# Kernel optimization log

Hardware: AMD Instinct MI355X
Metric: run time of the kernel (lower is better)

The kernel has to match this reference:

```python
import jax, jax.numpy as jnp
import numpy as np

BETA = 100.0


def setup_inputs() -> dict:
    key = jax.random.key(0)
    k1, k2 = jax.random.split(key)
    E, d, N = 1250000, 64, 50000
    M = jax.random.normal(k1, (E, d), dtype=jnp.float32)
    dest = jax.random.randint(k2, (E,), 0, N, dtype=jnp.int32)
    return {"M": M, "dest": dest, "dim_size": N}


def reference(M, dest, dim_size):
    # scatter_max over dim 0: per-node elementwise max of incoming messages -> [N, d]
    M_v = jax.ops.segment_max(M, dest, num_segments=dim_size)
    # scatter_softmax(M * BETA, dest): segment-wise stable softmax along dim 0
    logits = M * BETA  # [E, d]
    seg_max = jax.ops.segment_max(logits, dest, num_segments=dim_size)  # [N, d]
    z = jnp.exp(logits - seg_max[dest])  # [E, d]
    denom = jax.ops.segment_sum(z, dest, num_segments=dim_size)  # [N, d]
    w = (z / denom[dest])[:, None, :]  # unsqueeze(1) -> [E, 1, d]
    return (M_v, w)
```

## Files before the change

### kernel.cpp

```cpp
#include <hip/hip_runtime.h>
#include <cmath>

#define BETA 100.0f
#define CAP 80


__global__ void k_zero1(int* __restrict__ p, int n) {
    int i = blockIdx.x * blockDim.x + threadIdx.x;
    if (i < n) p[i] = 0;
}

__global__ void k_place(const int* __restrict__ dest, int* __restrict__ cursor,
                        int* __restrict__ bucket, int e, int cap) {
    int i = blockIdx.x * blockDim.x + threadIdx.x;
    if (i < e) {
        int d = dest[i];
        int pos = atomicAdd(&cursor[d], 1);
        if (pos < cap) bucket[d * cap + pos] = i;
    }
}

#define SCAN_B 128
#define SCAN_T 256

__global__ void k_zero(int* __restrict__ cnt, int* __restrict__ cursor, int n) {
    int i = blockIdx.x * blockDim.x + threadIdx.x;
    if (i < n) { cnt[i] = 0; cursor[i] = 0; }
}

__global__ void k_hist(const int* __restrict__ dest, int* __restrict__ cnt, int e) {
    int i = blockIdx.x * blockDim.x + threadIdx.x;
    if (i < e) atomicAdd(&cnt[dest[i]], 1);
}

__global__ void __launch_bounds__(SCAN_T) k_scan1(const int* __restrict__ cnt,
                                                  int* __restrict__ partial, int n) {
    int b = blockIdx.x, tid = threadIdx.x;
    int per_b = (n + SCAN_B - 1) / SCAN_B;
    int bs = b * per_b;
    int be = bs + per_b; if (be > n) be = n;
    int sum = 0;
    for (int i = bs + tid; i < be; i += SCAN_T) sum += cnt[i];
    __shared__ int lds[SCAN_T];
    lds[tid] = sum;
    __syncthreads();
    for (int off = SCAN_T >> 1; off > 0; off >>= 1) {
        if (tid < off) lds[tid] += lds[tid + off];
        __syncthreads();
    }
    if (tid == 0) partial[b] = lds[0];
}

__global__ void __launch_bounds__(SCAN_B) k_scan2(int* __restrict__ partial) {
    int tid = threadIdx.x;
    __shared__ int lds[SCAN_B];
    int v = partial[tid];
    lds[tid] = v;
    __syncthreads();
    for (int off = 1; off < SCAN_B; off <<= 1) {
        int t = (tid >= off) ? lds[tid - off] : 0;
        __syncthreads();
        lds[tid] += t;
        __syncthreads();
    }
    partial[tid] = lds[tid] - v;
}

__global__ void __launch_bounds__(SCAN_T) k_scan3(const int* __restrict__ cnt,
                                                  const int* __restrict__ partial,
                                                  int* __restrict__ offs, int n) {
    int b = blockIdx.x, tid = threadIdx.x;
    int per_b = (n + SCAN_B - 1) / SCAN_B;
    int bs = b * per_b;
    int be = bs + per_b; if (be > n) be = n;
    int per_t = (per_b + SCAN_T - 1) / SCAN_T;
    int ts = bs + tid * per_t;
    int te = ts + per_t; if (te > be) te = be;
    int sum = 0;
    for (int i = ts; i < te; ++i) sum += cnt[i];
    __shared__ int lds[SCAN_T];
    lds[tid] = sum;
    __syncthreads();
    for (int off = 1; off < SCAN_T; off <<= 1) {
        int t = (tid >= off) ? lds[tid - off] : 0;
        __syncthreads();
        lds[tid] += t;
        __syncthreads();
    }
    int run = partial[b] + lds[tid] - sum;
    for (int i = ts; i < te; ++i) { offs[i] = run; run += cnt[i]; }
}

__global__ void k_bucket(const int* __restrict__ dest, const int* __restrict__ offs,
                         int* __restrict__ cursor, int* __restrict__ bucket, int e) {
    int i = blockIdx.x * blockDim.x + threadIdx.x;
    if (i < e) {
        int d = dest[i];
        int pos = atomicAdd(&cursor[d], 1);
        bucket[offs[d] + pos] = i;
    }
}

__global__ void __launch_bounds__(256) k_node(const float4* __restrict__ M4,
                                              const int* __restrict__ cnt,
                                              const int* __restrict__ offs,
                                              const int* __restrict__ bucket,
                                              float4* __restrict__ mv4,
                                              float4* __restrict__ w4, int n, int stride) {
    int tid = threadIdx.x;
    int node = blockIdx.x * 4 + (tid >> 6);
    if (node >= n) return;
    int lane = tid & 63;
    int g = lane >> 4;
    int q = lane & 15;
    int count = cnt[node];
    int base;
    if (stride > 0) {
        if (count > stride) count = stride;
        base = node * stride;
    } else {
        base = offs[node];
    }

    if (count == 0) {
        if (g == 0) mv4[(size_t)node * 16 + q] =
            make_float4(-INFINITY, -INFINITY, -INFINITY, -INFINITY);
        return;
    }

    if (count <= 64) {
        int eL = bucket[base + (lane < count ? lane : 0)];

        float4 mx = make_float4(-INFINITY, -INFINITY, -INFINITY, -INFINITY);
        float4 s = make_float4(0.f, 0.f, 0.f, 0.f);
        #pragma unroll 2
        for (int j = 0; j < count; j += 4) {
            int jj = j + g;
            bool act = jj < count;
            int e = __shfl(eL, act ? jj : 0);
            float4 v = M4[(size_t)e * 16 + q];
            if (act) {
                float nm;
                nm = fmaxf(mx.x, v.x);
                s.x = s.x * __expf(BETA * (mx.x - nm)) + __expf(BETA * (v.x - nm));
                mx.x = nm;
                nm = fmaxf(mx.y, v.y);
                s.y = s.y * __expf(BETA * (mx.y - nm)) + __expf(BETA * (v.y - nm));
                mx.y = nm;
                nm = fmaxf(mx.z, v.z);
                s.z = s.z * __expf(BETA * (mx.z - nm)) + __expf(BETA * (v.z - nm));
                mx.z = nm;
                nm = fmaxf(mx.w, v.w);
                s.w = s.w * __expf(BETA * (mx.w - nm)) + __expf(BETA * (v.w - nm));
                mx.w = nm;
            }
        }
        #pragma unroll
        for (int off = 16; off <= 32; off <<= 1) {
            float om, os, nm;
            om = __shfl_xor(mx.x, off); os = __shfl_xor(s.x, off);
            nm = fmaxf(mx.x, om);
            s.x = s.x * __expf(BETA * (mx.x - nm)) + os * __expf(BETA * (om - nm));
            mx.x = nm;
            om = __shfl_xor(mx.y, off); os = __shfl_xor(s.y, off);
            nm = fmaxf(mx.y, om);
            s.y = s.y * __expf(BETA * (mx.y - nm)) + os * __expf(BETA * (om - nm));
            mx.y = nm;
            om = __shfl_xor(mx.z, off); os = __shfl_xor(s.z, off);
            nm = fmaxf(mx.z, om);
            s.z = s.z * __expf(BETA * (mx.z - nm)) + os * __expf(BETA * (om - nm));
            mx.z = nm;
            om = __shfl_xor(mx.w, off); os = __shfl_xor(s.w, off);
            nm = fmaxf(mx.w, om);
            s.w = s.w * __expf(BETA * (mx.w - nm)) + os * __expf(BETA * (om - nm));
            mx.w = nm;
        }
        float4 inv;
        inv.x = __builtin_amdgcn_rcpf(s.x);
        inv.y = __builtin_amdgcn_rcpf(s.y);
        inv.z = __builtin_amdgcn_rcpf(s.z);
        inv.w = __builtin_amdgcn_rcpf(s.w);

        #pragma unroll 2
        for (int j = 0; j < count; j += 4) {
            int jj = j + g;
            bool act = jj < count;
            int e = __shfl(eL, act ? jj : 0);
            float4 v = M4[(size_t)e * 16 + q];
            if (act) {
                float4 o;
                o.x = __expf(BETA * (v.x - mx.x)) * inv.x;
                o.y = __expf(BETA * (v.y - mx.y)) * inv.y;
                o.z = __expf(BETA * (v.z - mx.z)) * inv.z;
                o.w = __expf(BETA * (v.w - mx.w)) * inv.w;
                w4[(size_t)e * 16 + q] = o;
            }
        }
        if (g == 0) mv4[(size_t)node * 16 + q] = mx;
    } else {
        const float* M = (const float*)M4;
        float* mv = (float*)mv4;
        float* w = (float*)w4;
        float mxs = -INFINITY;
        for (int j = 0; j < count; ++j) {
            int e = bucket[base + j];
            mxs = fmaxf(mxs, M[(size_t)e * 64 + lane]);
        }
        float ss = 0.f;
        for (int j = 0; j < count; ++j) {
            int e = bucket[base + j];
            ss += __expf(BETA * (M[(size_t)e * 64 + lane] - mxs));
        }
        float invs = __builtin_amdgcn_rcpf(ss);
        for (int j = 0; j < count; ++j) {
            int e = bucket[base + j];
            float x = M[(size_t)e * 64 + lane];
            w[(size_t)e * 64 + lane] = __expf(BETA * (x - mxs)) * invs;
        }
        mv[(size_t)node * 64 + lane] = mxs;
    }
}

extern "C" void kernel_launch(void* const* d_in, const int* in_sizes, int n_in,
                              void* d_out, int out_size, void* d_ws, size_t ws_size,
                              hipStream_t stream) {
    const float* M = (const float*)d_in[0];
    const int* dest = (const int*)d_in[1];
    const int E = in_sizes[1];
    const int d = in_sizes[0] / E;
    const int N = (out_size - in_sizes[0]) / d;

    float* mv = (float*)d_out;
    float* w = (float*)d_out + (size_t)N * d;

    const int B = 256;
    size_t need_fast = ((size_t)N * (CAP + 1)) * sizeof(int);

    if (ws_size >= need_fast) {
        int* cursor = (int*)d_ws;
        int* bucket = cursor + N;
        hipLaunchKernelGGL(k_zero1, dim3((N + B - 1) / B), dim3(B), 0, stream, cursor, N);
        hipLaunchKernelGGL(k_place, dim3((E + B - 1) / B), dim3(B), 0, stream,
                           dest, cursor, bucket, E, CAP);
        hipLaunchKernelGGL(k_node, dim3((N + 3) / 4), dim3(B), 0, stream,
                           (const float4*)M, cursor, (const int*)nullptr, bucket,
                           (float4*)mv, (float4*)w, N, CAP);
    } else {
        int* cnt     = (int*)d_ws;
        int* cursor  = cnt + N;
        int* offs    = cursor + N;
        int* partial = offs + N;
        int* bucket  = partial + SCAN_B;
        hipLaunchKernelGGL(k_zero, dim3((N + B - 1) / B), dim3(B), 0, stream, cnt, cursor, N);
        hipLaunchKernelGGL(k_hist, dim3((E + B - 1) / B), dim3(B), 0, stream, dest, cnt, E);
        hipLaunchKernelGGL(k_scan1, dim3(SCAN_B), dim3(SCAN_T), 0, stream, cnt, partial, N);
        hipLaunchKernelGGL(k_scan2, dim3(1), dim3(SCAN_B), 0, stream, partial);
        hipLaunchKernelGGL(k_scan3, dim3(SCAN_B), dim3(SCAN_T), 0, stream, cnt, partial, offs, N);
        hipLaunchKernelGGL(k_bucket, dim3((E + B - 1) / B), dim3(B), 0, stream,
                           dest, offs, cursor, bucket, E);
        hipLaunchKernelGGL(k_node, dim3((N + 3) / 4), dim3(B), 0, stream,
                           (const float4*)M, cnt, offs, bucket, (float4*)mv, (float4*)w, N, 0);
    }
}
```

Baseline: 263.8 us.

## Add register-cached fast path for nodes with up to 32 incoming edges

For segments with at most 32 edges, each wave loads all messages once into a register array of eight float4s. It then computes the max with plain fmax, exponentiates once and sums, and writes the weights from the cached exponentials. This replaces the online-softmax loop, which re-read M in a second pass and evaluated exp three times per element. The fixed eight-slot array raises register pressure, which may lower occupancy.

```diff
diff --git a/kernel.cpp b/kernel.cpp
--- a/kernel.cpp
+++ b/kernel.cpp
@@ -128,9 +128,68 @@
         return;
     }
 
-    if (count <= 64) {
+    if (count <= 32) {
         int eL = bucket[base + (lane < count ? lane : 0)];
-
+        float4 vc[8];
+        #pragma unroll
+        for (int t = 0; t < 8; ++t) {
+            int jj = t * 4 + g;
+            bool act = jj < count;
+            int e = __shfl(eL, act ? jj : 0);
+            if (act) {
+                vc[t] = M4[(size_t)e * 16 + q];
+            } else {
+                vc[t] = make_float4(-INFINITY, -INFINITY, -INFINITY, -INFINITY);
+            }
+        }
+        float4 mx = vc[0];
+        #pragma unroll
+        for (int t = 1; t < 8; ++t) {
+            mx.x = fmaxf(mx.x, vc[t].x); mx.y = fmaxf(mx.y, vc[t].y);
+            mx.z = fmaxf(mx.z, vc[t].z); mx.w = fmaxf(mx.w, vc[t].w);
+        }
+        #pragma unroll
+        for (int off = 16; off <= 32; off <<= 1) {
+            mx.x = fmaxf(mx.x, __shfl_xor(mx.x, off));
+            mx.y = fmaxf(mx.y, __shfl_xor(mx.y, off));
+            mx.z = fmaxf(mx.z, __shfl_xor(mx.z, off));
+            mx.w = fmaxf(mx.w, __shfl_xor(mx.w, off));
+        }
+        float4 s = make_float4(0.f, 0.f, 0.f, 0.f);
+        #pragma unroll
+        for (int t = 0; t < 8; ++t) {
+            vc[t].x = __expf(BETA * (vc[t].x - mx.x)); s.x += vc[t].x;
+            vc[t].y = __expf(BETA * (vc[t].y - mx.y)); s.y += vc[t].y;
+            vc[t].z = __expf(BETA * (vc[t].z - mx.z)); s.z += vc[t].z;
+            vc[t].w = __expf(BETA * (vc[t].w - mx.w)); s.w += vc[t].w;
+        }
+        #pragma unroll
+        for (int off = 16; off <= 32; off <<= 1) {
+            s.x += __shfl_xor(s.x, off);
+            s.y += __shfl_xor(s.y, off);
+            s.z += __shfl_xor(s.z, off);
+            s.w += __shfl_xor(s.w, off);
+        }
+        float4 inv;
+        inv.x = __builtin_amdgcn_rcpf(s.x);
+        inv.y = __builtin_amdgcn_rcpf(s.y);
+        inv.z = __builtin_amdgcn_rcpf(s.z);
+        inv.w = __builtin_amdgcn_rcpf(s.w);
+        #pragma unroll
+        for (int t = 0; t < 8; ++t) {
+            int jj = t * 4 + g;
+            bool act = jj < count;
+            int e = __shfl(eL, act ? jj : 0);
+            if (act) {
+                float4 o;
+                o.x = vc[t].x * inv.x; o.y = vc[t].y * inv.y;
+                o.z = vc[t].z * inv.z; o.w = vc[t].w * inv.w;
+                w4[(size_t)e * 16 + q] = o;
+            }
+        }
+        if (g == 0) mv4[(size_t)node * 16 + q] = mx;
+    } else if (count <= 64) {
+        int eL = bucket[base + (lane < count ? lane : 0)];
         float4 mx = make_float4(-INFINITY, -INFINITY, -INFINITY, -INFINITY);
         float4 s = make_float4(0.f, 0.f, 0.f, 0.f);
         #pragma unroll 2
@@ -180,7 +239,6 @@
         inv.y = __builtin_amdgcn_rcpf(s.y);
         inv.z = __builtin_amdgcn_rcpf(s.z);
         inv.w = __builtin_amdgcn_rcpf(s.w);
-
         #pragma unroll 2
         for (int j = 0; j < count; j += 4) {
             int jj = j + g;
```

Result: faster. 252.3 us (-4.3%).
